# Performance work log

Hardware: AMD Instinct MI355X
Metric: run time of the kernel (lower is better)

## Reference

```python
import jax, jax.numpy as jnp
import numpy as np

N = 100000
E = 3200000
F_IN, H1, H2, C = 128, 64, 32, 10


def setup_inputs() -> dict:
    key = jax.random.key(0)
    ks = jax.random.split(key, 8)
    x = jax.random.normal(ks[0], (N, F_IN), dtype=jnp.float32)
    edge_index = jax.random.randint(ks[1], (2, E), 0, N, dtype=jnp.int64)
    W1 = jax.random.normal(ks[2], (F_IN, H1), dtype=jnp.float32) / np.sqrt(F_IN)
    b1 = jnp.zeros((H1,), dtype=jnp.float32)
    W2 = jax.random.normal(ks[3], (H1, H2), dtype=jnp.float32) / np.sqrt(H1)
    b2 = jnp.zeros((H2,), dtype=jnp.float32)
    Wc = jax.random.normal(ks[4], (H2, C), dtype=jnp.float32) / np.sqrt(H2)
    bc = jnp.zeros((C,), dtype=jnp.float32)
    return {"x": x, "edge_index": edge_index, "W1": W1, "b1": b1,
            "W2": W2, "b2": b2, "Wc": Wc, "bc": bc}


def gcn_conv(x, src, dst, W, b, n):
    # PyG GCNConv: x' = D^{-1/2} (A + I) D^{-1/2} (X W) + b
    h = x @ W                                        # [N, H]
    ones = jnp.ones((src.shape[0],), dtype=h.dtype)
    deg = jax.ops.segment_sum(ones, dst, num_segments=n) + 1.0  # +1 self loop
    dinv = jax.lax.rsqrt(deg)                        # deg >= 1, safe
    norm = dinv[src] * dinv[dst]                     # [E]
    msg = h[src] * norm[:, None]                     # [E, H] gather + scale
    agg = jax.ops.segment_sum(msg, dst, num_segments=n)
    # self-loop contribution: norm_ii = 1/deg_i
    out = agg + h * (dinv * dinv)[:, None]
    return out + b


def reference(x, edge_index, W1, b1, W2, b2, Wc, bc):
    n = x.shape[0]
    src, dst = edge_index[0], edge_index[1]
    h = gcn_conv(x, src, dst, W1, b1, n)
    h = jax.nn.relu(h)
    # dropout is identity in eval mode (training=False)
    h = gcn_conv(h, src, dst, W2, b2, n)
    h = jax.nn.relu(h)
    logits = h @ Wc + bc
    return jax.nn.log_softmax(logits, axis=1)
```

## Files before the change

kernel.cpp:

```cpp
#include <hip/hip_runtime.h>


#define BSHIFT 8
#define BMASK 255
#define NBUCK_MAX 512
#define TILE 4096
#define EPT 16

__device__ __forceinline__ unsigned pack_bf16(float lo, float hi) {
    unsigned ul = __float_as_uint(lo);
    ul = (ul + 0x7FFFu + ((ul >> 16) & 1u)) >> 16;
    unsigned uh = __float_as_uint(hi);
    uh = ((uh + 0x7FFFu + ((uh >> 16) & 1u)) >> 16) << 16;
    return ul | uh;
}

__global__ void k_hist(const int* __restrict__ dst, int* __restrict__ bcnt, int E) {
    __shared__ int h[NBUCK_MAX];
    for (int i = threadIdx.x; i < NBUCK_MAX; i += blockDim.x) h[i] = 0;
    __syncthreads();
    for (int e = blockIdx.x * blockDim.x + threadIdx.x; e < E; e += gridDim.x * blockDim.x)
        atomicAdd(&h[dst[e] >> BSHIFT], 1);
    __syncthreads();
    for (int i = threadIdx.x; i < NBUCK_MAX; i += blockDim.x)
        if (h[i]) atomicAdd(&bcnt[i], h[i]);
}

__global__ void k_scanb(const int* __restrict__ bcnt, int* __restrict__ bbase,
                        int* __restrict__ gcur, int E) {
    __shared__ int s[NBUCK_MAX];
    int t = threadIdx.x;
    int v = bcnt[t];
    s[t] = v;
    __syncthreads();
    for (int o = 1; o < NBUCK_MAX; o <<= 1) {
        int u = (t >= o) ? s[t - o] : 0;
        __syncthreads();
        s[t] += u;
        __syncthreads();
    }
    int ex = s[t] - v;
    bbase[t] = ex;
    gcur[t] = ex;
    if (t == NBUCK_MAX - 1) bbase[NBUCK_MAX] = E;
}

__global__ __launch_bounds__(256) void k_binA(const int* __restrict__ src,
                                              const int* __restrict__ dst,
                                              int* __restrict__ gcur,
                                              int* __restrict__ binned, int E) {
    __shared__ int hist[NBUCK_MAX];
    __shared__ int lbase[NBUCK_MAX];
    __shared__ int gdelta[NBUCK_MAX];
    __shared__ int cnt2[NBUCK_MAX];
    __shared__ int scanb[256];
    __shared__ int stage[TILE];
    __shared__ unsigned short sbucket[TILE];

    int t = threadIdx.x;
    for (int i = t; i < NBUCK_MAX; i += 256) { hist[i] = 0; cnt2[i] = 0; }
    __syncthreads();

    int tileStart = blockIdx.x * TILE;
    int cntTile = min(TILE, E - tileStart);

    int vals[EPT];
    int bks[EPT];
#pragma unroll
    for (int i = 0; i < EPT; i++) {
        int e = tileStart + t + i * 256;
        if (e < E) {
            int s = src[e], d = dst[e];
            vals[i] = s | ((d & BMASK) << 17);
            bks[i] = d >> BSHIFT;
            atomicAdd(&hist[bks[i]], 1);
        } else bks[i] = -1;
    }
    __syncthreads();

    int a0 = hist[2 * t], a1 = hist[2 * t + 1];
    int ts = a0 + a1;
    scanb[t] = ts;
    __syncthreads();
    for (int o = 1; o < 256; o <<= 1) {
        int u = (t >= o) ? scanb[t - o] : 0;
        __syncthreads();
        scanb[t] += u;
        __syncthreads();
    }
    int ex = scanb[t] - ts;
    lbase[2 * t] = ex;
    lbase[2 * t + 1] = ex + a0;
    __syncthreads();

    for (int b = t; b < NBUCK_MAX; b += 256) {
        int c = hist[b];
        int g = c ? atomicAdd(&gcur[b], c) : 0;
        gdelta[b] = g - lbase[b];
    }
#pragma unroll
    for (int i = 0; i < EPT; i++) {
        if (bks[i] >= 0) {
            int rr = atomicAdd(&cnt2[bks[i]], 1);
            int slot = lbase[bks[i]] + rr;
            stage[slot] = vals[i];
            sbucket[slot] = (unsigned short)bks[i];
        }
    }
    __syncthreads();
    for (int i = t; i < cntTile; i += 256) {
        int b = sbucket[i];
        binned[gdelta[b] + i] = stage[i];
    }
}

__global__ void k_sortcsr(const int* __restrict__ bbase, const int* __restrict__ binned,
                          int* __restrict__ rowptr, float* __restrict__ dinv,
                          int* __restrict__ csr, int n, int E) {
    __shared__ int cnt[256];
    __shared__ int sc[256];
    __shared__ int rpl[256];
    __shared__ int lcur[256];
    int b = blockIdx.x, t = threadIdx.x;
    cnt[t] = 0; lcur[t] = 0;
    __syncthreads();
    int beg = bbase[b], end = bbase[b + 1];
    for (int i = beg + t; i < end; i += 256)
        atomicAdd(&cnt[(binned[i] >> 17) & BMASK], 1);
    __syncthreads();
    int v = cnt[t];
    sc[t] = v;
    __syncthreads();
    for (int o = 1; o < 256; o <<= 1) {
        int u = (t >= o) ? sc[t - o] : 0;
        __syncthreads();
        sc[t] += u;
        __syncthreads();
    }
    int rp = beg + sc[t] - v;
    rpl[t] = rp;
    int g = (b << BSHIFT) + t;
    if (g < n) {
        rowptr[g] = rp;
        dinv[g] = rsqrtf((float)v + 1.0f);
        if (g == n - 1) rowptr[n] = E;
    }
    __syncthreads();
    for (int i = beg + t; i < end; i += 256) {
        int vv = binned[i];
        int ln = (vv >> 17) & BMASK;
        int k = atomicAdd(&lcur[ln], 1);
        csr[rpl[ln] + k] = vv & 0x1FFFF;
    }
}

template<int K, int M>
__global__ __launch_bounds__(256) void k_gemm(const float* __restrict__ X,
                                              const float* __restrict__ W,
                                              const float* __restrict__ dinv,
                                              unsigned* __restrict__ hsb, int n) {
    constexpr int MW = M / 4;
    __shared__ float Ws[K * M];
    for (int i = threadIdx.x; i < K * M; i += 256) Ws[i] = W[i];
    __syncthreads();
    int w = threadIdx.x >> 6, lane = threadIdx.x & 63;
    int wo = w * MW;
    int r0 = blockIdx.x * 256 + lane;
    float acc[4][MW];
#pragma unroll
    for (int i = 0; i < 4; i++)
#pragma unroll
        for (int j = 0; j < MW; j++) acc[i][j] = 0.f;

    for (int k = 0; k < K; k += 4) {
        float4 xv[4];
#pragma unroll
        for (int i = 0; i < 4; i++) {
            int rr = r0 + 64 * i;
            xv[i] = (rr < n) ? *(const float4*)(X + (size_t)rr * K + k)
                             : make_float4(0.f, 0.f, 0.f, 0.f);
        }
#pragma unroll
        for (int kk = 0; kk < 4; kk++) {
#pragma unroll
            for (int j = 0; j < MW; j += 4) {
                float4 wv = *(const float4*)&Ws[(k + kk) * M + wo + j];
#pragma unroll
                for (int i = 0; i < 4; i++) {
                    float xs = (kk == 0) ? xv[i].x : (kk == 1) ? xv[i].y
                             : (kk == 2) ? xv[i].z : xv[i].w;
                    acc[i][j + 0] += xs * wv.x;
                    acc[i][j + 1] += xs * wv.y;
                    acc[i][j + 2] += xs * wv.z;
                    acc[i][j + 3] += xs * wv.w;
                }
            }
        }
    }
#pragma unroll
    for (int i = 0; i < 4; i++) {
        int rr = r0 + 64 * i;
        if (rr < n) {
            float di = dinv[rr];
            unsigned p[MW / 2];
#pragma unroll
            for (int jj = 0; jj < MW / 2; jj++)
                p[jj] = pack_bf16(acc[i][2 * jj] * di, acc[i][2 * jj + 1] * di);
            unsigned* hr = hsb + (size_t)rr * (M / 2) + wo / 2;
#pragma unroll
            for (int jj = 0; jj < MW / 2; jj += 4)
                *(uint4*)(hr + jj) = make_uint4(p[jj], p[jj + 1], p[jj + 2], p[jj + 3]);
        }
    }
}

__global__ void k_agg64n(const int* __restrict__ rowptr, const int* __restrict__ csr,
                         const uint4* __restrict__ hsb, const float* __restrict__ dinv,
                         const float* __restrict__ bv, float* __restrict__ out, int n) {
    __shared__ float bs[64];
    if (threadIdx.x < 64) bs[threadIdx.x] = bv[threadIdx.x];
    __syncthreads();
    int d = (blockIdx.x * blockDim.x + threadIdx.x) >> 6;
    if (d >= n) return;
    int lane = threadIdx.x & 63;
    int q = lane >> 3;
    int r = lane & 7;
    int beg = rowptr[d], end = rowptr[d + 1];
    float acc[8];
#pragma unroll
    for (int i = 0; i < 8; i++) acc[i] = 0.f;
    int base = beg;
    for (; base + 16 <= end; base += 16) {
        int sA = csr[base + q];
        int sB = csr[base + 8 + q];
        uint4 wA = hsb[(size_t)sA * 8 + r];
        uint4 wB = hsb[(size_t)sB * 8 + r];
        acc[0] += __uint_as_float(wA.x << 16);  acc[1] += __uint_as_float(wA.x & 0xFFFF0000u);
        acc[2] += __uint_as_float(wA.y << 16);  acc[3] += __uint_as_float(wA.y & 0xFFFF0000u);
        acc[4] += __uint_as_float(wA.z << 16);  acc[5] += __uint_as_float(wA.z & 0xFFFF0000u);
        acc[6] += __uint_as_float(wA.w << 16);  acc[7] += __uint_as_float(wA.w & 0xFFFF0000u);
        acc[0] += __uint_as_float(wB.x << 16);  acc[1] += __uint_as_float(wB.x & 0xFFFF0000u);
        acc[2] += __uint_as_float(wB.y << 16);  acc[3] += __uint_as_float(wB.y & 0xFFFF0000u);
        acc[4] += __uint_as_float(wB.z << 16);  acc[5] += __uint_as_float(wB.z & 0xFFFF0000u);
        acc[6] += __uint_as_float(wB.w << 16);  acc[7] += __uint_as_float(wB.w & 0xFFFF0000u);
    }
    if (base + q < end) {
        uint4 w = hsb[(size_t)csr[base + q] * 8 + r];
        acc[0] += __uint_as_float(w.x << 16);  acc[1] += __uint_as_float(w.x & 0xFFFF0000u);
        acc[2] += __uint_as_float(w.y << 16);  acc[3] += __uint_as_float(w.y & 0xFFFF0000u);
        acc[4] += __uint_as_float(w.z << 16);  acc[5] += __uint_as_float(w.z & 0xFFFF0000u);
        acc[6] += __uint_as_float(w.w << 16);  acc[7] += __uint_as_float(w.w & 0xFFFF0000u);
    }
    if (base + 8 + q < end) {
        uint4 w = hsb[(size_t)csr[base + 8 + q] * 8 + r];
        acc[0] += __uint_as_float(w.x << 16);  acc[1] += __uint_as_float(w.x & 0xFFFF0000u);
        acc[2] += __uint_as_float(w.y << 16);  acc[3] += __uint_as_float(w.y & 0xFFFF0000u);
        acc[4] += __uint_as_float(w.z << 16);  acc[5] += __uint_as_float(w.z & 0xFFFF0000u);
        acc[6] += __uint_as_float(w.w << 16);  acc[7] += __uint_as_float(w.w & 0xFFFF0000u);
    }
#pragma unroll
    for (int i = 0; i < 8; i++) {
        acc[i] += __shfl_xor(acc[i], 8, 64);
        acc[i] += __shfl_xor(acc[i], 16, 64);
        acc[i] += __shfl_xor(acc[i], 32, 64);
    }
    uint4 ws = hsb[(size_t)d * 8 + r];
    acc[0] += __uint_as_float(ws.x << 16);  acc[1] += __uint_as_float(ws.x & 0xFFFF0000u);
    acc[2] += __uint_as_float(ws.y << 16);  acc[3] += __uint_as_float(ws.y & 0xFFFF0000u);
    acc[4] += __uint_as_float(ws.z << 16);  acc[5] += __uint_as_float(ws.z & 0xFFFF0000u);
    acc[6] += __uint_as_float(ws.w << 16);  acc[7] += __uint_as_float(ws.w & 0xFFFF0000u);
    if (q == 0) {
        float di = dinv[d];
        float v[8];
#pragma unroll
        for (int i = 0; i < 8; i++) v[i] = fmaxf(acc[i] * di + bs[8 * r + i], 0.f);
        float* o = out + (size_t)d * 64 + 8 * r;
        *(float4*)(o + 0) = make_float4(v[0], v[1], v[2], v[3]);
        *(float4*)(o + 4) = make_float4(v[4], v[5], v[6], v[7]);
    }
}

__global__ void k_agg32n(const int* __restrict__ rowptr, const int* __restrict__ csr,
                         const uint4* __restrict__ hsb, const float* __restrict__ dinv,
                         const float* __restrict__ bv, float* __restrict__ out, int n) {
    __shared__ float bs[32];
    if (threadIdx.x < 32) bs[threadIdx.x] = bv[threadIdx.x];
    __syncthreads();
    int d = (blockIdx.x * blockDim.x + threadIdx.x) >> 6;
    if (d >= n) return;
    int lane = threadIdx.x & 63;
    int q = lane >> 2;
    int r = lane & 3;
    int beg = rowptr[d], end = rowptr[d + 1];
    float acc[8];
#pragma unroll
    for (int i = 0; i < 8; i++) acc[i] = 0.f;
    int base = beg;
    for (; base + 32 <= end; base += 32) {
        int sA = csr[base + q];
        int sB = csr[base + 16 + q];
        uint4 wA = hsb[(size_t)sA * 4 + r];
        uint4 wB = hsb[(size_t)sB * 4 + r];
        acc[0] += __uint_as_float(wA.x << 16);  acc[1] += __uint_as_float(wA.x & 0xFFFF0000u);
        acc[2] += __uint_as_float(wA.y << 16);  acc[3] += __uint_as_float(wA.y & 0xFFFF0000u);
        acc[4] += __uint_as_float(wA.z << 16);  acc[5] += __uint_as_float(wA.z & 0xFFFF0000u);
        acc[6] += __uint_as_float(wA.w << 16);  acc[7] += __uint_as_float(wA.w & 0xFFFF0000u);
        acc[0] += __uint_as_float(wB.x << 16);  acc[1] += __uint_as_float(wB.x & 0xFFFF0000u);
        acc[2] += __uint_as_float(wB.y << 16);  acc[3] += __uint_as_float(wB.y & 0xFFFF0000u);
        acc[4] += __uint_as_float(wB.z << 16);  acc[5] += __uint_as_float(wB.z & 0xFFFF0000u);
        acc[6] += __uint_as_float(wB.w << 16);  acc[7] += __uint_as_float(wB.w & 0xFFFF0000u);
    }
    if (base + q < end) {
        uint4 w = hsb[(size_t)csr[base + q] * 4 + r];
        acc[0] += __uint_as_float(w.x << 16);  acc[1] += __uint_as_float(w.x & 0xFFFF0000u);
        acc[2] += __uint_as_float(w.y << 16);  acc[3] += __uint_as_float(w.y & 0xFFFF0000u);
        acc[4] += __uint_as_float(w.z << 16);  acc[5] += __uint_as_float(w.z & 0xFFFF0000u);
        acc[6] += __uint_as_float(w.w << 16);  acc[7] += __uint_as_float(w.w & 0xFFFF0000u);
    }
    if (base + 16 + q < end) {
        uint4 w = hsb[(size_t)csr[base + 16 + q] * 4 + r];
        acc[0] += __uint_as_float(w.x << 16);  acc[1] += __uint_as_float(w.x & 0xFFFF0000u);
        acc[2] += __uint_as_float(w.y << 16);  acc[3] += __uint_as_float(w.y & 0xFFFF0000u);
        acc[4] += __uint_as_float(w.z << 16);  acc[5] += __uint_as_float(w.z & 0xFFFF0000u);
        acc[6] += __uint_as_float(w.w << 16);  acc[7] += __uint_as_float(w.w & 0xFFFF0000u);
    }
#pragma unroll
    for (int i = 0; i < 8; i++) {
        acc[i] += __shfl_xor(acc[i], 4, 64);
        acc[i] += __shfl_xor(acc[i], 8, 64);
        acc[i] += __shfl_xor(acc[i], 16, 64);
        acc[i] += __shfl_xor(acc[i], 32, 64);
    }
    uint4 ws = hsb[(size_t)d * 4 + r];
    acc[0] += __uint_as_float(ws.x << 16);  acc[1] += __uint_as_float(ws.x & 0xFFFF0000u);
    acc[2] += __uint_as_float(ws.y << 16);  acc[3] += __uint_as_float(ws.y & 0xFFFF0000u);
    acc[4] += __uint_as_float(ws.z << 16);  acc[5] += __uint_as_float(ws.z & 0xFFFF0000u);
    acc[6] += __uint_as_float(ws.w << 16);  acc[7] += __uint_as_float(ws.w & 0xFFFF0000u);
    if (q == 0) {
        float di = dinv[d];
        float v[8];
#pragma unroll
        for (int i = 0; i < 8; i++) v[i] = fmaxf(acc[i] * di + bs[8 * r + i], 0.f);
        float* o = out + (size_t)d * 32 + 8 * r;
        *(float4*)(o + 0) = make_float4(v[0], v[1], v[2], v[3]);
        *(float4*)(o + 4) = make_float4(v[4], v[5], v[6], v[7]);
    }
}

__global__ void k_classifier(const float* __restrict__ ACT, const float* __restrict__ Wc,
                             const float* __restrict__ bc, float* __restrict__ out, int n) {
    __shared__ float Wcs[32 * 10];
    __shared__ float bcs[10];
    for (int i = threadIdx.x; i < 320; i += blockDim.x) Wcs[i] = Wc[i];
    if (threadIdx.x < 10) bcs[threadIdx.x] = bc[threadIdx.x];
    __syncthreads();
    int r = blockIdx.x * blockDim.x + threadIdx.x;
    if (r >= n) return;
    const float* a = ACT + (size_t)r * 32;
    float logits[10];
#pragma unroll
    for (int c = 0; c < 10; c++) logits[c] = bcs[c];
#pragma unroll
    for (int k = 0; k < 32; k += 4) {
        float4 av = *(const float4*)(a + k);
#pragma unroll
        for (int c = 0; c < 10; c++) {
            logits[c] += av.x * Wcs[(k + 0) * 10 + c] + av.y * Wcs[(k + 1) * 10 + c]
                       + av.z * Wcs[(k + 2) * 10 + c] + av.w * Wcs[(k + 3) * 10 + c];
        }
    }
    float m = logits[0];
#pragma unroll
    for (int c = 1; c < 10; c++) m = fmaxf(m, logits[c]);
    float ssum = 0.f;
#pragma unroll
    for (int c = 0; c < 10; c++) ssum += __expf(logits[c] - m);
    float lse = m + __logf(ssum);
    float* o = out + (size_t)r * 10;
#pragma unroll
    for (int c = 0; c < 10; c++) o[c] = logits[c] - lse;
}

extern "C" void kernel_launch(void* const* d_in, const int* in_sizes, int n_in,
                              void* d_out, int out_size, void* d_ws, size_t ws_size,
                              hipStream_t stream) {
    const float* x  = (const float*)d_in[0];
    const int*   ei = (const int*)d_in[1];
    const float* W1 = (const float*)d_in[2];
    const float* b1 = (const float*)d_in[3];
    const float* W2 = (const float*)d_in[4];
    const float* b2 = (const float*)d_in[5];
    const float* Wc = (const float*)d_in[6];
    const float* bc = (const float*)d_in[7];
    float* out = (float*)d_out;

    const int N = in_sizes[0] / 128;
    const int E = in_sizes[1] / 2;
    const int* src = ei;
    const int* dst = ei + E;

    const int NBUCK = (N + BMASK) >> BSHIFT;
    const int NTILE = (E + TILE - 1) / TILE;

    char* ws = (char*)d_ws;
    size_t off = 0;
    auto alloc = [&](size_t elems) {
        void* p = ws + off;
        off += ((elems * 4 + 1023) & ~(size_t)1023);
        return p;
    };
    float*    dinv   = (float*)alloc(N);
    int*      bcnt   = (int*)alloc(NBUCK_MAX);
    int*      bbase  = (int*)alloc(NBUCK_MAX + 1);
    int*      gcur   = (int*)alloc(NBUCK_MAX);
    int*      rowptr = (int*)alloc(N + 1);
    int*      binned = (int*)alloc(E);
    int*      csr    = (int*)alloc(E);
    unsigned* hsb    = (unsigned*)alloc((size_t)N * 32);
    float*    act    = (float*)alloc((size_t)N * 64);

    hipMemsetAsync(bcnt, 0, sizeof(int) * NBUCK_MAX, stream);

    k_hist<<<512, 256, 0, stream>>>(dst, bcnt, E);
    k_scanb<<<1, NBUCK_MAX, 0, stream>>>(bcnt, bbase, gcur, E);
    k_binA<<<NTILE, 256, 0, stream>>>(src, dst, gcur, binned, E);
    k_sortcsr<<<NBUCK, 256, 0, stream>>>(bbase, binned, rowptr, dinv, csr, N, E);

    k_gemm<128, 64><<<(N + 255) / 256, 256, 0, stream>>>(x, W1, dinv, hsb, N);
    k_agg64n<<<(N * 64 + 255) / 256, 256, 0, stream>>>(rowptr, csr, (const uint4*)hsb,
                                                       dinv, b1, act, N);

    k_gemm<64, 32><<<(N + 255) / 256, 256, 0, stream>>>(act, W2, dinv, hsb, N);
    k_agg32n<<<(N * 64 + 255) / 256, 256, 0, stream>>>(rowptr, csr, (const uint4*)hsb,
                                                       dinv, b2, act, N);

    k_classifier<<<(N + 255) / 256, 256, 0, stream>>>(act, Wc, bc, out, N);
}
```

Before: 376.7 us.

## Stage X tiles through double-buffered shared memory in dense GEMM kernel

The GEMM kernel now loads 128-row by 16-column tiles of X cooperatively into padded, double-buffered shared memory. The next tile is prefetched into registers while the current one is computed. Each block now covers 128 rows with 2 rows per thread instead of 256 rows with 4, which doubles the grid size. The aim is coalesced global reads of X instead of strided per-thread float4 row reads, plus load/compute overlap, at the cost of extra LDS traffic and one barrier per k-tile.

```diff
diff --git a/kernel.cpp b/kernel.cpp
--- a/kernel.cpp
+++ b/kernel.cpp
@@ -160,46 +160,72 @@
                                               const float* __restrict__ dinv,
                                               unsigned* __restrict__ hsb, int n) {
     constexpr int MW = M / 4;
+    constexpr int KT = 16;
+    constexpr int NT = K / KT;
+    constexpr int RS = KT + 4;
     __shared__ float Ws[K * M];
+    __shared__ float Xs[2][128 * RS];
     for (int i = threadIdx.x; i < K * M; i += 256) Ws[i] = W[i];
-    __syncthreads();
-    int w = threadIdx.x >> 6, lane = threadIdx.x & 63;
+
+    int t = threadIdx.x;
+    int w = t >> 6, lane = t & 63;
     int wo = w * MW;
-    int r0 = blockIdx.x * 256 + lane;
-    float acc[4][MW];
-#pragma unroll
-    for (int i = 0; i < 4; i++)
+    int rowBase = blockIdx.x * 128;
+
+    int srow0 = t >> 2, sch0 = t & 3;
+    int srow1 = (t + 256) >> 2, sch1 = t & 3;
+    float4 sreg0, sreg1;
+    auto gload = [&](int kt) {
+        int gr0 = rowBase + srow0, gr1 = rowBase + srow1;
+        sreg0 = (gr0 < n) ? *(const float4*)(X + (size_t)gr0 * K + kt * KT + sch0 * 4)
+                          : make_float4(0.f, 0.f, 0.f, 0.f);
+        sreg1 = (gr1 < n) ? *(const float4*)(X + (size_t)gr1 * K + kt * KT + sch1 * 4)
+                          : make_float4(0.f, 0.f, 0.f, 0.f);
+    };
+    auto swrite = [&](int b) {
+        *(float4*)&Xs[b][srow0 * RS + sch0 * 4] = sreg0;
+        *(float4*)&Xs[b][srow1 * RS + sch1 * 4] = sreg1;
+    };
+
+    float acc[2][MW];
+#pragma unroll
+    for (int i = 0; i < 2; i++)
 #pragma unroll
         for (int j = 0; j < MW; j++) acc[i][j] = 0.f;
 
-    for (int k = 0; k < K; k += 4) {
-        float4 xv[4];
-#pragma unroll
-        for (int i = 0; i < 4; i++) {
-            int rr = r0 + 64 * i;
-            xv[i] = (rr < n) ? *(const float4*)(X + (size_t)rr * K + k)
-                             : make_float4(0.f, 0.f, 0.f, 0.f);
-        }
-#pragma unroll
-        for (int kk = 0; kk < 4; kk++) {
-#pragma unroll
-            for (int j = 0; j < MW; j += 4) {
-                float4 wv = *(const float4*)&Ws[(k + kk) * M + wo + j];
-#pragma unroll
-                for (int i = 0; i < 4; i++) {
-                    float xs = (kk == 0) ? xv[i].x : (kk == 1) ? xv[i].y
-                             : (kk == 2) ? xv[i].z : xv[i].w;
-                    acc[i][j + 0] += xs * wv.x;
-                    acc[i][j + 1] += xs * wv.y;
-                    acc[i][j + 2] += xs * wv.z;
-                    acc[i][j + 3] += xs * wv.w;
+    gload(0);
+    swrite(0);
+    __syncthreads();
+
+    for (int kt = 0; kt < NT; kt++) {
+        if (kt + 1 < NT) gload(kt + 1);
+        int b = kt & 1;
+#pragma unroll
+        for (int k4 = 0; k4 < KT / 4; k4++) {
+            float4 x0 = *(const float4*)&Xs[b][lane * RS + k4 * 4];
+            float4 x1 = *(const float4*)&Xs[b][(lane + 64) * RS + k4 * 4];
+#pragma unroll
+            for (int kk = 0; kk < 4; kk++) {
+                int kabs = kt * KT + k4 * 4 + kk;
+                float xs0 = (kk == 0) ? x0.x : (kk == 1) ? x0.y : (kk == 2) ? x0.z : x0.w;
+                float xs1 = (kk == 0) ? x1.x : (kk == 1) ? x1.y : (kk == 2) ? x1.z : x1.w;
+#pragma unroll
+                for (int j = 0; j < MW; j += 4) {
+                    float4 wv = *(const float4*)&Ws[kabs * M + wo + j];
+                    acc[0][j + 0] += xs0 * wv.x;  acc[0][j + 1] += xs0 * wv.y;
+                    acc[0][j + 2] += xs0 * wv.z;  acc[0][j + 3] += xs0 * wv.w;
+                    acc[1][j + 0] += xs1 * wv.x;  acc[1][j + 1] += xs1 * wv.y;
+                    acc[1][j + 2] += xs1 * wv.z;  acc[1][j + 3] += xs1 * wv.w;
                 }
             }
         }
-    }
-#pragma unroll
-    for (int i = 0; i < 4; i++) {
-        int rr = r0 + 64 * i;
+        if (kt + 1 < NT) swrite((kt + 1) & 1);
+        __syncthreads();
+    }
+
+#pragma unroll
+    for (int i = 0; i < 2; i++) {
+        int rr = rowBase + 64 * i + lane;
         if (rr < n) {
             float di = dinv[rr];
             unsigned p[MW / 2];
@@ -426,11 +452,11 @@
     k_binA<<<NTILE, 256, 0, stream>>>(src, dst, gcur, binned, E);
     k_sortcsr<<<NBUCK, 256, 0, stream>>>(bbase, binned, rowptr, dinv, csr, N, E);
 
-    k_gemm<128, 64><<<(N + 255) / 256, 256, 0, stream>>>(x, W1, dinv, hsb, N);
+    k_gemm<128, 64><<<(N + 127) / 128, 256, 0, stream>>>(x, W1, dinv, hsb, N);
     k_agg64n<<<(N * 64 + 255) / 256, 256, 0, stream>>>(rowptr, csr, (const uint4*)hsb,
                                                        dinv, b1, act, N);
 
-    k_gemm<64, 32><<<(N + 255) / 256, 256, 0, stream>>>(act, W2, dinv, hsb, N);
+    k_gemm<64, 32><<<(N + 127) / 128, 256, 0, stream>>>(act, W2, dinv, hsb, N);
     k_agg32n<<<(N * 64 + 255) / 256, 256, 0, stream>>>(rowptr, csr, (const uint4*)hsb,
                                                        dinv, b2, act, N);
 
```

New measurement: 443.4 us. 1.18x slower.
